# Optimization experiments

Measured on AMD Instinct MI355X. Metric: run time of the kernel, lower is better.

The kernel has to match this reference:

```python
import jax, jax.numpy as jnp
import numpy as np

B, N, D = 2, 2048, 512
H, DH = 8, 64
P = 64  # position_max_embedding


def setup_inputs() -> dict:
    key = jax.random.key(0)
    ks = jax.random.split(key, 8)
    s = 0.02
    return {
        "x": jax.random.normal(ks[0], (B, N, D), jnp.float32),
        "Wq": jax.random.normal(ks[1], (D, H * DH), jnp.float32) * s,
        "Wk": jax.random.normal(ks[2], (D, H * DH), jnp.float32) * s,
        "Wv": jax.random.normal(ks[3], (D, H * DH), jnp.float32) * s,
        "rel_pos": jax.random.normal(ks[4], (2 * P + 1, H), jnp.float32) * s,
        "c_emb": jax.random.uniform(ks[5], (2 * P + 1, H), jnp.float32, 0.5, 1.5),
        "Wo": jax.random.normal(ks[6], (H * DH, D), jnp.float32) * s,
        "bo": jnp.zeros((D,), jnp.float32),
    }


def reference(x, Wq, Wk, Wv, rel_pos, c_emb, Wo, bo):
    b, n, _ = x.shape
    scale = DH ** -0.5
    q = (x @ Wq).reshape(b, n, H, DH)
    k = (x @ Wk).reshape(b, n, H, DH)
    v = (x @ Wv).reshape(b, n, H, DH)
    # relative position index: j - i, clamped to [-P, P], shifted to [0, 2P]
    idx = jnp.clip(jnp.arange(n)[None, :] - jnp.arange(n)[:, None], -P, P) + P  # [n, n]
    pos_bias = rel_pos[idx]          # [n, n, H]
    c_gate = c_emb[idx]              # [n, n, H]
    sim = jnp.einsum('bihd,bjhd->bhij', q, k)  # [b, H, n, n]
    sim = (sim + pos_bias.transpose(2, 0, 1)[None]) * scale
    attn = jax.nn.softmax(sim, axis=-1) * c_gate.transpose(2, 0, 1)[None]
    out = jnp.einsum('bhij,bjhd->bihd', attn, v).reshape(b, n, H * DH)
    return out @ Wo + bo
```

## Files before the change

### kernel.cpp

```cpp
#include <hip/hip_runtime.h>
#include <stdint.h>

#define BB 2
#define NN 2048
#define DD 512
#define HH 8
#define DHH 64

typedef __attribute__((ext_vector_type(8))) short bf16x8;
typedef __attribute__((ext_vector_type(4))) float f32x4;

#define LOG2E 1.44269504088896340736f

#if __has_builtin(__builtin_amdgcn_exp2f)
#define QSCALE (0.125f * LOG2E)
#define EXP2(x) __builtin_amdgcn_exp2f(x)
#else
#define QSCALE 0.125f
#define EXP2(x) __expf(x)
#endif

static __device__ __forceinline__ unsigned short f2bf(float f) {
    union { float f; unsigned u; } v; v.f = f;
    unsigned r = v.u + 0x7fffu + ((v.u >> 16) & 1u);
    return (unsigned short)(r >> 16);
}

static __device__ __forceinline__ unsigned pkbf(float a, float b) {
    union { float f; unsigned u; } ua, ub; ua.f = a; ub.f = b;
    return ((ub.u + 0x8000u) & 0xffff0000u) | ((ua.u + 0x8000u) >> 16);
}

static __device__ __forceinline__ bf16x8 ld8(const unsigned short* p) {
    bf16x8 v; __builtin_memcpy(&v, p, 16); return v;
}

static __device__ __forceinline__ void gld_lds16(const void* g, void* l) {
    __builtin_amdgcn_global_load_lds((const __attribute__((address_space(1))) void*)g,
                                     (__attribute__((address_space(3))) void*)l, 16, 0, 0);
}

__global__ void ca_prep(const float* __restrict__ x,
                        const float* __restrict__ w0, const float* __restrict__ w1,
                        const float* __restrict__ w2, const float* __restrict__ w3,
                        unsigned short* __restrict__ xb, unsigned short* __restrict__ wts) {
    __shared__ float T[64][65];
    int bx = blockIdx.x;
    if (bx < 2048) {
        int gid = bx * 256 + threadIdx.x;
        float4 v = ((const float4*)x)[gid];
        ushort4 o;
        o.x = f2bf(v.x); o.y = f2bf(v.y); o.z = f2bf(v.z); o.w = f2bf(v.w);
        ((ushort4*)xb)[gid] = o;
        return;
    }
    int bb = bx - 2048;
    int z = bb >> 6, t = bb & 63;
    const float* W = (z == 0) ? w0 : (z == 1) ? w1 : (z == 2) ? w2 : w3;
    unsigned short* out = wts + z * 262144;
    int k0 = (t & 7) << 6, n0 = (t >> 3) << 6;
    int c = threadIdx.x & 63, r4 = threadIdx.x >> 6;
#pragma unroll
    for (int rr = 0; rr < 16; ++rr) {
        int r = r4 * 16 + rr;
        T[r][c] = W[(k0 + r) * 512 + n0 + c];
    }
    __syncthreads();
#pragma unroll
    for (int rr = 0; rr < 16; ++rr) {
        int r = r4 * 16 + rr;
        out[(n0 + r) * 512 + k0 + c] = f2bf(T[c][r]);
    }
}

__global__ __launch_bounds__(256, 3)
void ca_gemm_proj(const unsigned short* __restrict__ A,
                  const unsigned short* __restrict__ wts,
                  unsigned short* __restrict__ qkv,
                  unsigned short* __restrict__ vt) {
    __shared__ __align__(16) unsigned short Ash[2][128 * 64];
    __shared__ __align__(16) unsigned short Bsh[2][64 * 64];
    int z = blockIdx.y >> 3;
    const unsigned short* BT = wts + z * 262144;
    unsigned short* out = qkv + z * 2097152;
    int w = threadIdx.x >> 6, lane = threadIdx.x & 63;
    int c = lane & 15, qd = lane >> 4;
    int m0 = blockIdx.x * 128 + w * 16;
    int n0 = (blockIdx.y & 7) * 64;

    int lr = lane >> 3, ls = lane & 7;
    int soff = lr * 512 + ((ls ^ (lr & 7)) << 3);
    const unsigned short* Ab = A + (blockIdx.x * 128) * 512 + soff;
    const unsigned short* Bb = BT + n0 * 512 + soff;

#pragma unroll
    for (int L = 0; L < 4; ++L)
        gld_lds16(Ab + (w * 32 + L * 8) * 512, (char*)Ash[0] + (w * 32 + L * 8) * 128);
#pragma unroll
    for (int L = 0; L < 2; ++L)
        gld_lds16(Bb + (w * 16 + L * 8) * 512, (char*)Bsh[0] + (w * 16 + L * 8) * 128);

    f32x4 acc[2][4];
#pragma unroll
    for (int mt = 0; mt < 2; ++mt)
#pragma unroll
        for (int nb = 0; nb < 4; ++nb) acc[mt][nb] = (f32x4){0.f, 0.f, 0.f, 0.f};

    int cs = c & 7;
#pragma unroll
    for (int k = 0; k < 8; ++k) {
        int b = k & 1;
        if (k < 7) {
            int k0 = (k + 1) * 64;
#pragma unroll
            for (int L = 0; L < 4; ++L)
                gld_lds16(Ab + k0 + (w * 32 + L * 8) * 512, (char*)Ash[b ^ 1] + (w * 32 + L * 8) * 128);
#pragma unroll
            for (int L = 0; L < 2; ++L)
                gld_lds16(Bb + k0 + (w * 16 + L * 8) * 512, (char*)Bsh[b ^ 1] + (w * 16 + L * 8) * 128);
            asm volatile("s_waitcnt vmcnt(6)" ::: "memory");
        } else {
            asm volatile("s_waitcnt vmcnt(0)" ::: "memory");
        }
        __syncthreads();
        bf16x8 a[2][2], bq[4][2];
#pragma unroll
        for (int mt = 0; mt < 2; ++mt)
#pragma unroll
            for (int kk = 0; kk < 2; ++kk)
                a[mt][kk] = ld8((const unsigned short*)((char*)Ash[b] +
                                (w * 16 + mt * 64 + c) * 128 + (((kk * 4 + qd) ^ cs) << 4)));
#pragma unroll
        for (int nb = 0; nb < 4; ++nb)
#pragma unroll
            for (int kk = 0; kk < 2; ++kk)
                bq[nb][kk] = ld8((const unsigned short*)((char*)Bsh[b] +
                                (nb * 16 + c) * 128 + (((kk * 4 + qd) ^ cs) << 4)));
        asm volatile("s_waitcnt lgkmcnt(0)" ::: "memory");
        __syncthreads();
#pragma unroll
        for (int kk = 0; kk < 2; ++kk)
#pragma unroll
            for (int nb = 0; nb < 4; ++nb) {
                acc[0][nb] = __builtin_amdgcn_mfma_f32_16x16x32_bf16(a[0][kk], bq[nb][kk], acc[0][nb], 0, 0, 0);
                acc[1][nb] = __builtin_amdgcn_mfma_f32_16x16x32_bf16(a[1][kk], bq[nb][kk], acc[1][nb], 0, 0, 0);
            }
    }

    if (z == 2) {
#pragma unroll
        for (int mt = 0; mt < 2; ++mt) {
            int ib = m0 + mt * 64 + qd * 4;
            int b = ib >> 11, i = ib & 2047;
#pragma unroll
            for (int nb = 0; nb < 4; ++nb) {
                int col = n0 + nb * 16 + c;
                int h = col >> 6, d = col & 63;
                ushort4 pk;
                pk.x = f2bf(acc[mt][nb][0]); pk.y = f2bf(acc[mt][nb][1]);
                pk.z = f2bf(acc[mt][nb][2]); pk.w = f2bf(acc[mt][nb][3]);
                *(ushort4*)(vt + (((b << 3) + h) * 64 + d) * 2048 + i) = pk;
            }
        }
    } else {
        float scale = (z == 0) ? QSCALE : 1.0f;
#pragma unroll
        for (int mt = 0; mt < 2; ++mt)
#pragma unroll
            for (int nb = 0; nb < 4; ++nb) {
#pragma unroll
                for (int r = 0; r < 4; ++r) {
                    int row = m0 + mt * 64 + qd * 4 + r;
                    int col = n0 + nb * 16 + c;
                    int b = row >> 11, i = row & 2047, h = col >> 6, d = col & 63;
                    out[(((b << 3) + h) * 2048 + i) * 64 + d] = f2bf(acc[mt][nb][r] * scale);
                }
            }
    }
}

__global__ __launch_bounds__(256, 4)
void ca_flash(const unsigned short* __restrict__ Q,
              const unsigned short* __restrict__ K,
              const unsigned short* __restrict__ VT,
              const float* __restrict__ rel_pos,
              const float* __restrict__ c_emb,
              unsigned short* __restrict__ Ob) {
    __shared__ __align__(16) char smem[37904];
    unsigned (*Ptu)[16][16] = (unsigned (*)[16][16])(smem + 32768);
    float* red = (float*)smem;
    float2* lrg = (float2*)(smem + 36864);

    int bx = blockIdx.x;
    int xcd = bx & 7, slot = bx >> 3;
    int bh = xcd + ((slot >> 6) << 3);
    int it = slot & 63;
    int b = bh >> 3, h = bh & 7;
    int w = threadIdx.x >> 6, lane = threadIdx.x & 63;
    int c = lane & 15, qd = lane >> 4;
    int i0 = it * 32;

    if (threadIdx.x < 129) {
        lrg[threadIdx.x] = make_float2(rel_pos[threadIdx.x * 8 + h] * QSCALE,
                                       c_emb[threadIdx.x * 8 + h]);
    }

    const unsigned short* Qh = Q  + bh * 131072;
    const unsigned short* Kh = K  + bh * 131072;
    const unsigned short* Vh = VT + bh * 131072;
    char* kw = smem + w * 4096;
    char* vw = smem + 16384 + w * 4096;

    int koff[4], voff[4];
#pragma unroll
    for (int L = 0; L < 4; ++L) {
        int kr = L * 8 + (lane >> 3);
        koff[L] = kr * 64 + (((lane & 7) ^ ((kr >> 1) & 7)) << 3);
        int vr = L * 16 + (lane >> 2);
        voff[L] = vr * 2048 + (((lane & 3) ^ ((lane >> 3) & 3)) << 3);
    }

    {
        int j0 = w * 32;
#pragma unroll
        for (int L = 0; L < 4; ++L) gld_lds16(Kh + j0 * 64 + koff[L], kw + L * 1024);
#pragma unroll
        for (int L = 0; L < 4; ++L) gld_lds16(Vh + j0 + voff[L], vw + L * 1024);
    }

    bf16x8 aq[2][2];
#pragma unroll
    for (int qt = 0; qt < 2; ++qt) {
        aq[qt][0] = ld8(Qh + (i0 + qt * 16 + c) * 64 + qd * 8);
        aq[qt][1] = ld8(Qh + (i0 + qt * 16 + c) * 64 + 32 + qd * 8);
    }

    f32x4 o2[2][4];
    float lp2[2][4];
#pragma unroll
    for (int qt = 0; qt < 2; ++qt)
#pragma unroll
        for (int db = 0; db < 4; ++db) {
            o2[qt][db] = (f32x4){0.f, 0.f, 0.f, 0.f};
            lp2[qt][db] = 0.f;
        }

    __syncthreads();

    int ksw  = c & 7;
    int vsw  = (c >> 1) & 3;

    for (int t = 0; t < 16; ++t) {
        asm volatile("s_waitcnt vmcnt(0)" ::: "memory");
        __builtin_amdgcn_sched_barrier(0);
        bf16x8 bk0a = ld8((const unsigned short*)(kw + (2 * c) * 128     + (((qd)     ^ ksw) << 4)));
        bf16x8 bk0b = ld8((const unsigned short*)(kw + (2 * c) * 128     + (((qd + 4) ^ ksw) << 4)));
        bf16x8 bk1a = ld8((const unsigned short*)(kw + (2 * c + 1) * 128 + (((qd)     ^ ksw) << 4)));
        bf16x8 bk1b = ld8((const unsigned short*)(kw + (2 * c + 1) * 128 + (((qd + 4) ^ ksw) << 4)));
        bf16x8 bv[4];
#pragma unroll
        for (int db = 0; db < 4; ++db)
            bv[db] = ld8((const unsigned short*)(vw + (db * 16 + c) * 64 + ((qd ^ vsw) << 4)));
        asm volatile("s_waitcnt lgkmcnt(0)" ::: "memory");
        __builtin_amdgcn_sched_barrier(0);
        if (t < 15) {
            int j0n = ((t + 1) * 4 + w) * 32;
#pragma unroll
            for (int L = 0; L < 4; ++L) gld_lds16(Kh + j0n * 64 + koff[L], kw + L * 1024);
#pragma unroll
            for (int L = 0; L < 4; ++L) gld_lds16(Vh + j0n + voff[L], vw + L * 1024);
        }

        int j0 = (t * 4 + w) * 32;
#pragma unroll
        for (int qt = 0; qt < 2; ++qt) {
            f32x4 s0 = (f32x4){0.f, 0.f, 0.f, 0.f};
            f32x4 s1 = (f32x4){0.f, 0.f, 0.f, 0.f};
            s0 = __builtin_amdgcn_mfma_f32_16x16x32_bf16(aq[qt][0], bk0a, s0, 0, 0, 0);
            s0 = __builtin_amdgcn_mfma_f32_16x16x32_bf16(aq[qt][1], bk0b, s0, 0, 0, 0);
            s1 = __builtin_amdgcn_mfma_f32_16x16x32_bf16(aq[qt][0], bk1a, s1, 0, 0, 0);
            s1 = __builtin_amdgcn_mfma_f32_16x16x32_bf16(aq[qt][1], bk1b, s1, 0, 0, 0);

            int iqt0 = i0 + qt * 16;
            int iq = iqt0 + qd * 4;
            bool lowc  = (j0 + 31 - iqt0) <= -64;
            bool highc = (j0 - (iqt0 + 15)) >= 64;
            if (lowc || highc) {
                int d = lowc ? 0 : 128;
                float2 gg = lrg[d];
#pragma unroll
                for (int r = 0; r < 4; ++r) {
                    float t0 = EXP2(s0[r] + gg.x);
                    float t1 = EXP2(s1[r] + gg.x);
                    lp2[qt][r] += t0 + t1;
                    Ptu[w][qd * 4 + r][c] = pkbf(t0 * gg.y, t1 * gg.y);
                }
            } else {
#pragma unroll
                for (int r = 0; r < 4; ++r) {
                    int i = iq + r;
                    int j = j0 + 2 * c;
                    int d0 = j - i;     d0 = (d0 < -64) ? -64 : (d0 > 64 ? 64 : d0); d0 += 64;
                    int d1 = j + 1 - i; d1 = (d1 < -64) ? -64 : (d1 > 64 ? 64 : d1); d1 += 64;
                    float2 g0 = lrg[d0];
                    float2 g1 = lrg[d1];
                    float t0 = EXP2(s0[r] + g0.x);
                    float t1 = EXP2(s1[r] + g1.x);
                    lp2[qt][r] += t0 + t1;
                    Ptu[w][qd * 4 + r][c] = pkbf(t0 * g0.y, t1 * g1.y);
                }
            }
            bf16x8 ap = ld8((const unsigned short*)&Ptu[w][c][0] + qd * 8);
#pragma unroll
            for (int db = 0; db < 4; ++db)
                o2[qt][db] = __builtin_amdgcn_mfma_f32_16x16x32_bf16(ap, bv[db], o2[qt][db], 0, 0, 0);
        }
    }

    __syncthreads();
    if (w > 0) {
        float* dst = red + (w - 1) * (64 * 41) + lane * 41;
#pragma unroll
        for (int qt = 0; qt < 2; ++qt)
#pragma unroll
            for (int db = 0; db < 4; ++db)
#pragma unroll
                for (int r = 0; r < 4; ++r)
                    dst[qt * 16 + db * 4 + r] = o2[qt][db][r];
#pragma unroll
        for (int qt = 0; qt < 2; ++qt)
#pragma unroll
            for (int r = 0; r < 4; ++r)
                dst[32 + qt * 4 + r] = lp2[qt][r];
    }
    __syncthreads();
    if (w == 0) {
#pragma unroll
        for (int ww = 0; ww < 3; ++ww) {
            const float* src = red + ww * (64 * 41) + lane * 41;
#pragma unroll
            for (int qt = 0; qt < 2; ++qt) {
#pragma unroll
                for (int db = 0; db < 4; ++db)
#pragma unroll
                    for (int r = 0; r < 4; ++r)
                        o2[qt][db][r] += src[qt * 16 + db * 4 + r];
#pragma unroll
                for (int r = 0; r < 4; ++r)
                    lp2[qt][r] += src[32 + qt * 4 + r];
            }
        }
#pragma unroll
        for (int qt = 0; qt < 2; ++qt)
#pragma unroll
            for (int r = 0; r < 4; ++r) {
                lp2[qt][r] += __shfl_xor(lp2[qt][r], 1);
                lp2[qt][r] += __shfl_xor(lp2[qt][r], 2);
                lp2[qt][r] += __shfl_xor(lp2[qt][r], 4);
                lp2[qt][r] += __shfl_xor(lp2[qt][r], 8);
            }
#pragma unroll
        for (int qt = 0; qt < 2; ++qt)
#pragma unroll
            for (int db = 0; db < 4; ++db)
#pragma unroll
                for (int r = 0; r < 4; ++r) {
                    int row = b * 2048 + i0 + qt * 16 + qd * 4 + r;
                    int col = h * 64 + db * 16 + c;
                    Ob[row * 512 + col] = f2bf(o2[qt][db][r] / lp2[qt][r]);
                }
    }
}

__global__ __launch_bounds__(256, 4)
void ca_gemm_out(const unsigned short* __restrict__ A,
                 const unsigned short* __restrict__ BT,
                 const float* __restrict__ bias,
                 float* __restrict__ out) {
    __shared__ __align__(16) unsigned short Ash[2][64 * 64];
    __shared__ __align__(16) unsigned short Bsh[2][64 * 64];
    int w = threadIdx.x >> 6, lane = threadIdx.x & 63;
    int c = lane & 15, qd = lane >> 4;
    int m0 = blockIdx.x * 64 + w * 16;
    int n0 = blockIdx.y * 64;

    int lr = lane >> 3, ls = lane & 7;
    int soff = lr * 512 + ((ls ^ (lr & 7)) << 3);
    const unsigned short* Ab = A + (blockIdx.x * 64) * 512 + soff;
    const unsigned short* Bb = BT + n0 * 512 + soff;

#pragma unroll
    for (int L = 0; L < 2; ++L) {
        gld_lds16(Ab + (w * 16 + L * 8) * 512, (char*)Ash[0] + (w * 16 + L * 8) * 128);
        gld_lds16(Bb + (w * 16 + L * 8) * 512, (char*)Bsh[0] + (w * 16 + L * 8) * 128);
    }

    f32x4 acc[4];
#pragma unroll
    for (int nb = 0; nb < 4; ++nb) acc[nb] = (f32x4){0.f, 0.f, 0.f, 0.f};

    int cs = c & 7;
#pragma unroll
    for (int k = 0; k < 8; ++k) {
        int b = k & 1;
        if (k < 7) {
            int k0 = (k + 1) * 64;
#pragma unroll
            for (int L = 0; L < 2; ++L) {
                gld_lds16(Ab + k0 + (w * 16 + L * 8) * 512, (char*)Ash[b ^ 1] + (w * 16 + L * 8) * 128);
                gld_lds16(Bb + k0 + (w * 16 + L * 8) * 512, (char*)Bsh[b ^ 1] + (w * 16 + L * 8) * 128);
            }
            asm volatile("s_waitcnt vmcnt(4)" ::: "memory");
        } else {
            asm volatile("s_waitcnt vmcnt(0)" ::: "memory");
        }
        __syncthreads();
        bf16x8 a[2], bq[4][2];
#pragma unroll
        for (int kk = 0; kk < 2; ++kk)
            a[kk] = ld8((const unsigned short*)((char*)Ash[b] +
                        (w * 16 + c) * 128 + (((kk * 4 + qd) ^ cs) << 4)));
#pragma unroll
        for (int nb = 0; nb < 4; ++nb)
#pragma unroll
            for (int kk = 0; kk < 2; ++kk)
                bq[nb][kk] = ld8((const unsigned short*)((char*)Bsh[b] +
                                (nb * 16 + c) * 128 + (((kk * 4 + qd) ^ cs) << 4)));
        asm volatile("s_waitcnt lgkmcnt(0)" ::: "memory");
        __syncthreads();
#pragma unroll
        for (int kk = 0; kk < 2; ++kk)
#pragma unroll
            for (int nb = 0; nb < 4; ++nb)
                acc[nb] = __builtin_amdgcn_mfma_f32_16x16x32_bf16(a[kk], bq[nb][kk], acc[nb], 0, 0, 0);
    }
#pragma unroll
    for (int nb = 0; nb < 4; ++nb) {
#pragma unroll
        for (int r = 0; r < 4; ++r) {
            int row = m0 + qd * 4 + r;
            int col = n0 + nb * 16 + c;
            out[row * 512 + col] = acc[nb][r] + bias[col];
        }
    }
}

extern "C" void kernel_launch(void* const* d_in, const int* in_sizes, int n_in,
                              void* d_out, int out_size, void* d_ws, size_t ws_size,
                              hipStream_t stream) {
    const float* x   = (const float*)d_in[0];
    const float* Wq  = (const float*)d_in[1];
    const float* Wk  = (const float*)d_in[2];
    const float* Wv  = (const float*)d_in[3];
    const float* rel = (const float*)d_in[4];
    const float* cem = (const float*)d_in[5];
    const float* Wo  = (const float*)d_in[6];
    const float* bo  = (const float*)d_in[7];
    float* out = (float*)d_out;
    char* ws = (char*)d_ws;

    unsigned short* xb  = (unsigned short*)(ws);
    unsigned short* wts = (unsigned short*)(ws + 4194304);
    unsigned short* qkv = (unsigned short*)(ws + 6291456);
    unsigned short* vt  = (unsigned short*)(ws + 18874368);
    unsigned short* ob  = (unsigned short*)(ws + 23068672);

    hipLaunchKernelGGL(ca_prep, dim3(2304), dim3(256), 0, stream, x, Wq, Wk, Wv, Wo, xb, wts);
    hipLaunchKernelGGL(ca_gemm_proj, dim3(32, 24), dim3(256), 0, stream, xb, wts, qkv, vt);
    hipLaunchKernelGGL(ca_flash, dim3(1024), dim3(256), 0, stream,
                       qkv, qkv + 2097152, vt, rel, cem, ob);
    hipLaunchKernelGGL(ca_gemm_out, dim3(64, 8), dim3(256), 0, stream, ob, wts + 3 * 262144, bo, out);
}
```

Baseline: 139.2 us.

## Merge four kernels into two using software grid barriers

Folds the prep/convert stage and the QKV projection GEMM into one persistent kernel separated by an atomic grid barrier. It likewise fuses the flash attention stage with the output projection GEMM in a second kernel with its own barrier, so launches drop from four to two plus a memset. The goal is to remove launch gaps and kernel-boundary drains. The cost is that the spin barriers require every block to be co-resident (768 and 1024 blocks) and could deadlock or serialize if occupancy is insufficient. It also adds a memset launch and barrier spin overhead.

```diff
diff --git a/kernel.cpp b/kernel.cpp
--- a/kernel.cpp
+++ b/kernel.cpp
@@ -40,407 +40,438 @@
                                      (__attribute__((address_space(3))) void*)l, 16, 0, 0);
 }
 
-__global__ void ca_prep(const float* __restrict__ x,
-                        const float* __restrict__ w0, const float* __restrict__ w1,
-                        const float* __restrict__ w2, const float* __restrict__ w3,
-                        unsigned short* __restrict__ xb, unsigned short* __restrict__ wts) {
-    __shared__ float T[64][65];
-    int bx = blockIdx.x;
-    if (bx < 2048) {
-        int gid = bx * 256 + threadIdx.x;
-        float4 v = ((const float4*)x)[gid];
-        ushort4 o;
-        o.x = f2bf(v.x); o.y = f2bf(v.y); o.z = f2bf(v.z); o.w = f2bf(v.w);
-        ((ushort4*)xb)[gid] = o;
-        return;
-    }
-    int bb = bx - 2048;
-    int z = bb >> 6, t = bb & 63;
-    const float* W = (z == 0) ? w0 : (z == 1) ? w1 : (z == 2) ? w2 : w3;
-    unsigned short* out = wts + z * 262144;
-    int k0 = (t & 7) << 6, n0 = (t >> 3) << 6;
-    int c = threadIdx.x & 63, r4 = threadIdx.x >> 6;
-#pragma unroll
-    for (int rr = 0; rr < 16; ++rr) {
-        int r = r4 * 16 + rr;
-        T[r][c] = W[(k0 + r) * 512 + n0 + c];
+static __device__ __forceinline__ void grid_barrier(unsigned* cnt, unsigned n) {
+    __syncthreads();
+    if (threadIdx.x == 0) {
+        __threadfence();
+        atomicAdd(cnt, 1u);
+        while (__hip_atomic_load(cnt, __ATOMIC_RELAXED, __HIP_MEMORY_SCOPE_AGENT) < n) {
+            __builtin_amdgcn_s_sleep(1);
+        }
+        __threadfence();
     }
     __syncthreads();
-#pragma unroll
-    for (int rr = 0; rr < 16; ++rr) {
-        int r = r4 * 16 + rr;
-        out[(n0 + r) * 512 + k0 + c] = f2bf(T[c][r]);
+}
+
+__global__ __launch_bounds__(256, 3)
+void ca_k1(const float* __restrict__ x,
+           const float* __restrict__ w0, const float* __restrict__ w1,
+           const float* __restrict__ w2, const float* __restrict__ w3,
+           unsigned short* __restrict__ xb, unsigned short* __restrict__ wts,
+           unsigned short* __restrict__ qkv, unsigned short* __restrict__ vt,
+           unsigned* __restrict__ bar) {
+    __shared__ __align__(16) char sm[49152];
+    int tid = threadIdx.x;
+
+    {
+        float (*T)[65] = (float (*)[65])sm;
+        for (int u = blockIdx.x; u < 2304; u += 768) {
+            if (u < 2048) {
+                int gid = u * 256 + tid;
+                float4 v = ((const float4*)x)[gid];
+                ushort4 o;
+                o.x = f2bf(v.x); o.y = f2bf(v.y); o.z = f2bf(v.z); o.w = f2bf(v.w);
+                ((ushort4*)xb)[gid] = o;
+            } else {
+                int bb = u - 2048;
+                int z = bb >> 6, t = bb & 63;
+                const float* W = (z == 0) ? w0 : (z == 1) ? w1 : (z == 2) ? w2 : w3;
+                unsigned short* out = wts + z * 262144;
+                int k0 = (t & 7) << 6, n0 = (t >> 3) << 6;
+                int c = tid & 63, r4 = tid >> 6;
+#pragma unroll
+                for (int rr = 0; rr < 16; ++rr) {
+                    int r = r4 * 16 + rr;
+                    T[r][c] = W[(k0 + r) * 512 + n0 + c];
+                }
+                __syncthreads();
+#pragma unroll
+                for (int rr = 0; rr < 16; ++rr) {
+                    int r = r4 * 16 + rr;
+                    out[(n0 + r) * 512 + k0 + c] = f2bf(T[c][r]);
+                }
+            }
+        }
     }
-}
-
-__global__ __launch_bounds__(256, 3)
-void ca_gemm_proj(const unsigned short* __restrict__ A,
-                  const unsigned short* __restrict__ wts,
-                  unsigned short* __restrict__ qkv,
-                  unsigned short* __restrict__ vt) {
-    __shared__ __align__(16) unsigned short Ash[2][128 * 64];
-    __shared__ __align__(16) unsigned short Bsh[2][64 * 64];
-    int z = blockIdx.y >> 3;
-    const unsigned short* BT = wts + z * 262144;
-    unsigned short* out = qkv + z * 2097152;
-    int w = threadIdx.x >> 6, lane = threadIdx.x & 63;
-    int c = lane & 15, qd = lane >> 4;
-    int m0 = blockIdx.x * 128 + w * 16;
-    int n0 = (blockIdx.y & 7) * 64;
-
-    int lr = lane >> 3, ls = lane & 7;
-    int soff = lr * 512 + ((ls ^ (lr & 7)) << 3);
-    const unsigned short* Ab = A + (blockIdx.x * 128) * 512 + soff;
-    const unsigned short* Bb = BT + n0 * 512 + soff;
-
-#pragma unroll
-    for (int L = 0; L < 4; ++L)
-        gld_lds16(Ab + (w * 32 + L * 8) * 512, (char*)Ash[0] + (w * 32 + L * 8) * 128);
-#pragma unroll
-    for (int L = 0; L < 2; ++L)
-        gld_lds16(Bb + (w * 16 + L * 8) * 512, (char*)Bsh[0] + (w * 16 + L * 8) * 128);
-
-    f32x4 acc[2][4];
-#pragma unroll
-    for (int mt = 0; mt < 2; ++mt)
-#pragma unroll
-        for (int nb = 0; nb < 4; ++nb) acc[mt][nb] = (f32x4){0.f, 0.f, 0.f, 0.f};
-
-    int cs = c & 7;
-#pragma unroll
-    for (int k = 0; k < 8; ++k) {
-        int b = k & 1;
-        if (k < 7) {
-            int k0 = (k + 1) * 64;
-#pragma unroll
-            for (int L = 0; L < 4; ++L)
-                gld_lds16(Ab + k0 + (w * 32 + L * 8) * 512, (char*)Ash[b ^ 1] + (w * 32 + L * 8) * 128);
-#pragma unroll
-            for (int L = 0; L < 2; ++L)
-                gld_lds16(Bb + k0 + (w * 16 + L * 8) * 512, (char*)Bsh[b ^ 1] + (w * 16 + L * 8) * 128);
-            asm volatile("s_waitcnt vmcnt(6)" ::: "memory");
+    grid_barrier(bar, 768);
+
+    {
+        char* AshB = sm;
+        char* BshB = sm + 32768;
+        int px = blockIdx.x & 31, py = blockIdx.x >> 5;
+        int z = py >> 3;
+        const unsigned short* BT = wts + z * 262144;
+        unsigned short* out = qkv + z * 2097152;
+        int w = tid >> 6, lane = tid & 63;
+        int c = lane & 15, qd = lane >> 4;
+        int m0 = px * 128 + w * 16;
+        int n0 = (py & 7) * 64;
+
+        int lr = lane >> 3, ls = lane & 7;
+        int soff = lr * 512 + ((ls ^ (lr & 7)) << 3);
+        const unsigned short* Ab = xb + (px * 128) * 512 + soff;
+        const unsigned short* Bb = BT + n0 * 512 + soff;
+
+#pragma unroll
+        for (int L = 0; L < 4; ++L)
+            gld_lds16(Ab + (w * 32 + L * 8) * 512, AshB + (w * 32 + L * 8) * 128);
+#pragma unroll
+        for (int L = 0; L < 2; ++L)
+            gld_lds16(Bb + (w * 16 + L * 8) * 512, BshB + (w * 16 + L * 8) * 128);
+
+        f32x4 acc[2][4];
+#pragma unroll
+        for (int mt = 0; mt < 2; ++mt)
+#pragma unroll
+            for (int nb = 0; nb < 4; ++nb) acc[mt][nb] = (f32x4){0.f, 0.f, 0.f, 0.f};
+
+        int cs = c & 7;
+#pragma unroll
+        for (int k = 0; k < 8; ++k) {
+            int b = k & 1;
+            if (k < 7) {
+                int k0 = (k + 1) * 64;
+#pragma unroll
+                for (int L = 0; L < 4; ++L)
+                    gld_lds16(Ab + k0 + (w * 32 + L * 8) * 512,
+                              AshB + (b ^ 1) * 16384 + (w * 32 + L * 8) * 128);
+#pragma unroll
+                for (int L = 0; L < 2; ++L)
+                    gld_lds16(Bb + k0 + (w * 16 + L * 8) * 512,
+                              BshB + (b ^ 1) * 8192 + (w * 16 + L * 8) * 128);
+                asm volatile("s_waitcnt vmcnt(6)" ::: "memory");
+            } else {
+                asm volatile("s_waitcnt vmcnt(0)" ::: "memory");
+            }
+            __syncthreads();
+            bf16x8 a[2][2], bq[4][2];
+#pragma unroll
+            for (int mt = 0; mt < 2; ++mt)
+#pragma unroll
+                for (int kk = 0; kk < 2; ++kk)
+                    a[mt][kk] = ld8((const unsigned short*)(AshB + b * 16384 +
+                                    (w * 16 + mt * 64 + c) * 128 + (((kk * 4 + qd) ^ cs) << 4)));
+#pragma unroll
+            for (int nb = 0; nb < 4; ++nb)
+#pragma unroll
+                for (int kk = 0; kk < 2; ++kk)
+                    bq[nb][kk] = ld8((const unsigned short*)(BshB + b * 8192 +
+                                     (nb * 16 + c) * 128 + (((kk * 4 + qd) ^ cs) << 4)));
+            asm volatile("s_waitcnt lgkmcnt(0)" ::: "memory");
+            __syncthreads();
+#pragma unroll
+            for (int kk = 0; kk < 2; ++kk)
+#pragma unroll
+                for (int nb = 0; nb < 4; ++nb) {
+                    acc[0][nb] = __builtin_amdgcn_mfma_f32_16x16x32_bf16(a[0][kk], bq[nb][kk], acc[0][nb], 0, 0, 0);
+                    acc[1][nb] = __builtin_amdgcn_mfma_f32_16x16x32_bf16(a[1][kk], bq[nb][kk], acc[1][nb], 0, 0, 0);
+                }
+        }
+
+        if (z == 2) {
+#pragma unroll
+            for (int mt = 0; mt < 2; ++mt) {
+                int ib = m0 + mt * 64 + qd * 4;
+                int b = ib >> 11, i = ib & 2047;
+#pragma unroll
+                for (int nb = 0; nb < 4; ++nb) {
+                    int col = n0 + nb * 16 + c;
+                    int h = col >> 6, d = col & 63;
+                    ushort4 pk;
+                    pk.x = f2bf(acc[mt][nb][0]); pk.y = f2bf(acc[mt][nb][1]);
+                    pk.z = f2bf(acc[mt][nb][2]); pk.w = f2bf(acc[mt][nb][3]);
+                    *(ushort4*)(vt + (((b << 3) + h) * 64 + d) * 2048 + i) = pk;
+                }
+            }
         } else {
+            float scale = (z == 0) ? QSCALE : 1.0f;
+#pragma unroll
+            for (int mt = 0; mt < 2; ++mt)
+#pragma unroll
+                for (int nb = 0; nb < 4; ++nb) {
+#pragma unroll
+                    for (int r = 0; r < 4; ++r) {
+                        int row = m0 + mt * 64 + qd * 4 + r;
+                        int col = n0 + nb * 16 + c;
+                        int b = row >> 11, i = row & 2047, h = col >> 6, d = col & 63;
+                        out[(((b << 3) + h) * 2048 + i) * 64 + d] = f2bf(acc[mt][nb][r] * scale);
+                    }
+                }
+        }
+    }
+}
+
+__global__ __launch_bounds__(256, 4)
+void ca_k2(const unsigned short* __restrict__ Q,
+           const unsigned short* __restrict__ K,
+           const unsigned short* __restrict__ VTp,
+           const float* __restrict__ rel_pos,
+           const float* __restrict__ c_emb,
+           unsigned short* __restrict__ Ob,
+           const unsigned short* __restrict__ WoT,
+           const float* __restrict__ bias,
+           float* __restrict__ out,
+           unsigned* __restrict__ bar) {
+    __shared__ __align__(16) char smem[37904];
+    int tid = threadIdx.x;
+
+    {
+        unsigned (*Ptu)[16][16] = (unsigned (*)[16][16])(smem + 32768);
+        float* red = (float*)smem;
+        float2* lrg = (float2*)(smem + 36864);
+
+        int bx = blockIdx.x;
+        int xcd = bx & 7, slot = bx >> 3;
+        int bh = xcd + ((slot >> 6) << 3);
+        int it = slot & 63;
+        int b = bh >> 3, h = bh & 7;
+        int w = tid >> 6, lane = tid & 63;
+        int c = lane & 15, qd = lane >> 4;
+        int i0 = it * 32;
+
+        if (tid < 129) {
+            lrg[tid] = make_float2(rel_pos[tid * 8 + h] * QSCALE, c_emb[tid * 8 + h]);
+        }
+
+        const unsigned short* Qh = Q   + bh * 131072;
+        const unsigned short* Kh = K   + bh * 131072;
+        const unsigned short* Vh = VTp + bh * 131072;
+        char* kw = smem + w * 4096;
+        char* vw = smem + 16384 + w * 4096;
+
+        int koff[4], voff[4];
+#pragma unroll
+        for (int L = 0; L < 4; ++L) {
+            int kr = L * 8 + (lane >> 3);
+            koff[L] = kr * 64 + (((lane & 7) ^ ((kr >> 1) & 7)) << 3);
+            int vr = L * 16 + (lane >> 2);
+            voff[L] = vr * 2048 + (((lane & 3) ^ ((lane >> 3) & 3)) << 3);
+        }
+
+        {
+            int j0 = w * 32;
+#pragma unroll
+            for (int L = 0; L < 4; ++L) gld_lds16(Kh + j0 * 64 + koff[L], kw + L * 1024);
+#pragma unroll
+            for (int L = 0; L < 4; ++L) gld_lds16(Vh + j0 + voff[L], vw + L * 1024);
+        }
+
+        bf16x8 aq[2][2];
+#pragma unroll
+        for (int qt = 0; qt < 2; ++qt) {
+            aq[qt][0] = ld8(Qh + (i0 + qt * 16 + c) * 64 + qd * 8);
+            aq[qt][1] = ld8(Qh + (i0 + qt * 16 + c) * 64 + 32 + qd * 8);
+        }
+
+        f32x4 o2[2][4];
+        float lp2[2][4];
+#pragma unroll
+        for (int qt = 0; qt < 2; ++qt)
+#pragma unroll
+            for (int db = 0; db < 4; ++db) {
+                o2[qt][db] = (f32x4){0.f, 0.f, 0.f, 0.f};
+                lp2[qt][db] = 0.f;
+            }
+
+        __syncthreads();
+
+        int ksw = c & 7;
+        int vsw = (c >> 1) & 3;
+
+        for (int t = 0; t < 16; ++t) {
             asm volatile("s_waitcnt vmcnt(0)" ::: "memory");
-        }
+            __builtin_amdgcn_sched_barrier(0);
+            bf16x8 bk0a = ld8((const unsigned short*)(kw + (2 * c) * 128     + (((qd)     ^ ksw) << 4)));
+            bf16x8 bk0b = ld8((const unsigned short*)(kw + (2 * c) * 128     + (((qd + 4) ^ ksw) << 4)));
+            bf16x8 bk1a = ld8((const unsigned short*)(kw + (2 * c + 1) * 128 + (((qd)     ^ ksw) << 4)));
+            bf16x8 bk1b = ld8((const unsigned short*)(kw + (2 * c + 1) * 128 + (((qd + 4) ^ ksw) << 4)));
+            bf16x8 bv[4];
+#pragma unroll
+            for (int db = 0; db < 4; ++db)
+                bv[db] = ld8((const unsigned short*)(vw + (db * 16 + c) * 64 + ((qd ^ vsw) << 4)));
+            asm volatile("s_waitcnt lgkmcnt(0)" ::: "memory");
+            __builtin_amdgcn_sched_barrier(0);
+            if (t < 15) {
+                int j0n = ((t + 1) * 4 + w) * 32;
+#pragma unroll
+                for (int L = 0; L < 4; ++L) gld_lds16(Kh + j0n * 64 + koff[L], kw + L * 1024);
+#pragma unroll
+                for (int L = 0; L < 4; ++L) gld_lds16(Vh + j0n + voff[L], vw + L * 1024);
+            }
+
+            int j0 = (t * 4 + w) * 32;
+#pragma unroll
+            for (int qt = 0; qt < 2; ++qt) {
+                f32x4 s0 = (f32x4){0.f, 0.f, 0.f, 0.f};
+                f32x4 s1 = (f32x4){0.f, 0.f, 0.f, 0.f};
+                s0 = __builtin_amdgcn_mfma_f32_16x16x32_bf16(aq[qt][0], bk0a, s0, 0, 0, 0);
+                s0 = __builtin_amdgcn_mfma_f32_16x16x32_bf16(aq[qt][1], bk0b, s0, 0, 0, 0);
+                s1 = __builtin_amdgcn_mfma_f32_16x16x32_bf16(aq[qt][0], bk1a, s1, 0, 0, 0);
+                s1 = __builtin_amdgcn_mfma_f32_16x16x32_bf16(aq[qt][1], bk1b, s1, 0, 0, 0);
+
+                int iqt0 = i0 + qt * 16;
+                int iq = iqt0 + qd * 4;
+                bool lowc  = (j0 + 31 - iqt0) <= -64;
+                bool highc = (j0 - (iqt0 + 15)) >= 64;
+                if (lowc || highc) {
+                    int d = lowc ? 0 : 128;
+                    float2 gg = lrg[d];
+#pragma unroll
+                    for (int r = 0; r < 4; ++r) {
+                        float t0 = EXP2(s0[r] + gg.x);
+                        float t1 = EXP2(s1[r] + gg.x);
+                        lp2[qt][r] += t0 + t1;
+                        Ptu[w][qd * 4 + r][c] = pkbf(t0 * gg.y, t1 * gg.y);
+                    }
+                } else {
+#pragma unroll
+                    for (int r = 0; r < 4; ++r) {
+                        int i = iq + r;
+                        int j = j0 + 2 * c;
+                        int d0 = j - i;     d0 = (d0 < -64) ? -64 : (d0 > 64 ? 64 : d0); d0 += 64;
+                        int d1 = j + 1 - i; d1 = (d1 < -64) ? -64 : (d1 > 64 ? 64 : d1); d1 += 64;
+                        float2 g0 = lrg[d0];
+                        float2 g1 = lrg[d1];
+                        float t0 = EXP2(s0[r] + g0.x);
+                        float t1 = EXP2(s1[r] + g1.x);
+                        lp2[qt][r] += t0 + t1;
+                        Ptu[w][qd * 4 + r][c] = pkbf(t0 * g0.y, t1 * g1.y);
+                    }
+                }
+                bf16x8 ap = ld8((const unsigned short*)&Ptu[w][c][0] + qd * 8);
+#pragma unroll
+                for (int db = 0; db < 4; ++db)
+                    o2[qt][db] = __builtin_amdgcn_mfma_f32_16x16x32_bf16(ap, bv[db], o2[qt][db], 0, 0, 0);
+            }
+        }
+
         __syncthreads();
-        bf16x8 a[2][2], bq[4][2];
-#pragma unroll
-        for (int mt = 0; mt < 2; ++mt)
+        if (w > 0) {
+            float* dst = red + (w - 1) * (64 * 41) + lane * 41;
+#pragma unroll
+            for (int qt = 0; qt < 2; ++qt)
+#pragma unroll
+                for (int db = 0; db < 4; ++db)
+#pragma unroll
+                    for (int r = 0; r < 4; ++r)
+                        dst[qt * 16 + db * 4 + r] = o2[qt][db][r];
+#pragma unroll
+            for (int qt = 0; qt < 2; ++qt)
+#pragma unroll
+                for (int r = 0; r < 4; ++r)
+                    dst[32 + qt * 4 + r] = lp2[qt][r];
+        }
+        __syncthreads();
+        if (w == 0) {
+#pragma unroll
+            for (int ww = 0; ww < 3; ++ww) {
+                const float* src = red + ww * (64 * 41) + lane * 41;
+#pragma unroll
+                for (int qt = 0; qt < 2; ++qt) {
+#pragma unroll
+                    for (int db = 0; db < 4; ++db)
+#pragma unroll
+                        for (int r = 0; r < 4; ++r)
+                            o2[qt][db][r] += src[qt * 16 + db * 4 + r];
+#pragma unroll
+                    for (int r = 0; r < 4; ++r)
+                        lp2[qt][r] += src[32 + qt * 4 + r];
+                }
+            }
+#pragma unroll
+            for (int qt = 0; qt < 2; ++qt)
+#pragma unroll
+                for (int r = 0; r < 4; ++r) {
+                    lp2[qt][r] += __shfl_xor(lp2[qt][r], 1);
+                    lp2[qt][r] += __shfl_xor(lp2[qt][r], 2);
+                    lp2[qt][r] += __shfl_xor(lp2[qt][r], 4);
+                    lp2[qt][r] += __shfl_xor(lp2[qt][r], 8);
+                }
+#pragma unroll
+            for (int qt = 0; qt < 2; ++qt)
+#pragma unroll
+                for (int db = 0; db < 4; ++db)
+#pragma unroll
+                    for (int r = 0; r < 4; ++r) {
+                        int row = b * 2048 + i0 + qt * 16 + qd * 4 + r;
+                        int col = h * 64 + db * 16 + c;
+                        Ob[row * 512 + col] = f2bf(o2[qt][db][r] / lp2[qt][r]);
+                    }
+        }
+    }
+
+    grid_barrier(bar, 1024);
+
+    if (blockIdx.x < 512) {
+        char* AshB = smem;
+        char* BshB = smem + 16384;
+        int u = blockIdx.x;
+        int px = u & 63, py = u >> 6;
+        int w = tid >> 6, lane = tid & 63;
+        int c = lane & 15, qd = lane >> 4;
+        int m0 = px * 64 + w * 16;
+        int n0 = py * 64;
+
+        int lr = lane >> 3, ls = lane & 7;
+        int soff = lr * 512 + ((ls ^ (lr & 7)) << 3);
+        const unsigned short* Ab = Ob + (px * 64) * 512 + soff;
+        const unsigned short* Bb = WoT + n0 * 512 + soff;
+
+#pragma unroll
+        for (int L = 0; L < 2; ++L) {
+            gld_lds16(Ab + (w * 16 + L * 8) * 512, AshB + (w * 16 + L * 8) * 128);
+            gld_lds16(Bb + (w * 16 + L * 8) * 512, BshB + (w * 16 + L * 8) * 128);
+        }
+
+        f32x4 acc[4];
+#pragma unroll
+        for (int nb = 0; nb < 4; ++nb) acc[nb] = (f32x4){0.f, 0.f, 0.f, 0.f};
+
+        int cs = c & 7;
+#pragma unroll
+        for (int k = 0; k < 8; ++k) {
+            int b = k & 1;
+            if (k < 7) {
+                int k0 = (k + 1) * 64;
+#pragma unroll
+                for (int L = 0; L < 2; ++L) {
+                    gld_lds16(Ab + k0 + (w * 16 + L * 8) * 512,
+                              AshB + (b ^ 1) * 8192 + (w * 16 + L * 8) * 128);
+                    gld_lds16(Bb + k0 + (w * 16 + L * 8) * 512,
+                              BshB + (b ^ 1) * 8192 + (w * 16 + L * 8) * 128);
+                }
+                asm volatile("s_waitcnt vmcnt(4)" ::: "memory");
+            } else {
+                asm volatile("s_waitcnt vmcnt(0)" ::: "memory");
+            }
+            __syncthreads();
+            bf16x8 a[2], bq[4][2];
 #pragma unroll
             for (int kk = 0; kk < 2; ++kk)
-                a[mt][kk] = ld8((const unsigned short*)((char*)Ash[b] +
-                                (w * 16 + mt * 64 + c) * 128 + (((kk * 4 + qd) ^ cs) << 4)));
-#pragma unroll
-        for (int nb = 0; nb < 4; ++nb)
+                a[kk] = ld8((const unsigned short*)(AshB + b * 8192 +
+                            (w * 16 + c) * 128 + (((kk * 4 + qd) ^ cs) << 4)));
+#pragma unroll
+            for (int nb = 0; nb < 4; ++nb)
+#pragma unroll
+                for (int kk = 0; kk < 2; ++kk)
+                    bq[nb][kk] = ld8((const unsigned short*)(BshB + b * 8192 +
+                                     (nb * 16 + c) * 128 + (((kk * 4 + qd) ^ cs) << 4)));
+            asm volatile("s_waitcnt lgkmcnt(0)" ::: "memory");
+            __syncthreads();
 #pragma unroll
             for (int kk = 0; kk < 2; ++kk)
-                bq[nb][kk] = ld8((const unsigned short*)((char*)Bsh[b] +
-                                (nb * 16 + c) * 128 + (((kk * 4 + qd) ^ cs) << 4)));
-        asm volatile("s_waitcnt lgkmcnt(0)" ::: "memory");
-        __syncthreads();
-#pragma unroll
-        for (int kk = 0; kk < 2; ++kk)
-#pragma unroll
-            for (int nb = 0; nb < 4; ++nb) {
-                acc[0][nb] = __builtin_amdgcn_mfma_f32_16x16x32_bf16(a[0][kk], bq[nb][kk], acc[0][nb], 0, 0, 0);
-                acc[1][nb] = __builtin_amdgcn_mfma_f32_16x16x32_bf16(a[1][kk], bq[nb][kk], acc[1][nb], 0, 0, 0);
-            }
-    }
-
-    if (z == 2) {
-#pragma unroll
-        for (int mt = 0; mt < 2; ++mt) {
-            int ib = m0 + mt * 64 + qd * 4;
-            int b = ib >> 11, i = ib & 2047;
-#pragma unroll
-            for (int nb = 0; nb < 4; ++nb) {
+#pragma unroll
+                for (int nb = 0; nb < 4; ++nb)
+                    acc[nb] = __builtin_amdgcn_mfma_f32_16x16x32_bf16(a[kk], bq[nb][kk], acc[nb], 0, 0, 0);
+        }
+#pragma unroll
+        for (int nb = 0; nb < 4; ++nb) {
+#pragma unroll
+            for (int r = 0; r < 4; ++r) {
+                int row = m0 + qd * 4 + r;
                 int col = n0 + nb * 16 + c;
-                int h = col >> 6, d = col & 63;
-                ushort4 pk;
-                pk.x = f2bf(acc[mt][nb][0]); pk.y = f2bf(acc[mt][nb][1]);
-                pk.z = f2bf(acc[mt][nb][2]); pk.w = f2bf(acc[mt][nb][3]);
-                *(ushort4*)(vt + (((b << 3) + h) * 64 + d) * 2048 + i) = pk;
-            }
-        }
-    } else {
-        float scale = (z == 0) ? QSCALE : 1.0f;
-#pragma unroll
-        for (int mt = 0; mt < 2; ++mt)
-#pragma unroll
-            for (int nb = 0; nb < 4; ++nb) {
-#pragma unroll
-                for (int r = 0; r < 4; ++r) {
-                    int row = m0 + mt * 64 + qd * 4 + r;
-                    int col = n0 + nb * 16 + c;
-                    int b = row >> 11, i = row & 2047, h = col >> 6, d = col & 63;
-                    out[(((b << 3) + h) * 2048 + i) * 64 + d] = f2bf(acc[mt][nb][r] * scale);
-                }
-            }
-    }
-}
-
-__global__ __launch_bounds__(256, 4)
-void ca_flash(const unsigned short* __restrict__ Q,
-              const unsigned short* __restrict__ K,
-              const unsigned short* __restrict__ VT,
-              const float* __restrict__ rel_pos,
-              const float* __restrict__ c_emb,
-              unsigned short* __restrict__ Ob) {
-    __shared__ __align__(16) char smem[37904];
-    unsigned (*Ptu)[16][16] = (unsigned (*)[16][16])(smem + 32768);
-    float* red = (float*)smem;
-    float2* lrg = (float2*)(smem + 36864);
-
-    int bx = blockIdx.x;
-    int xcd = bx & 7, slot = bx >> 3;
-    int bh = xcd + ((slot >> 6) << 3);
-    int it = slot & 63;
-    int b = bh >> 3, h = bh & 7;
-    int w = threadIdx.x >> 6, lane = threadIdx.x & 63;
-    int c = lane & 15, qd = lane >> 4;
-    int i0 = it * 32;
-
-    if (threadIdx.x < 129) {
-        lrg[threadIdx.x] = make_float2(rel_pos[threadIdx.x * 8 + h] * QSCALE,
-                                       c_emb[threadIdx.x * 8 + h]);
-    }
-
-    const unsigned short* Qh = Q  + bh * 131072;
-    const unsigned short* Kh = K  + bh * 131072;
-    const unsigned short* Vh = VT + bh * 131072;
-    char* kw = smem + w * 4096;
-    char* vw = smem + 16384 + w * 4096;
-
-    int koff[4], voff[4];
-#pragma unroll
-    for (int L = 0; L < 4; ++L) {
-        int kr = L * 8 + (lane >> 3);
-        koff[L] = kr * 64 + (((lane & 7) ^ ((kr >> 1) & 7)) << 3);
-        int vr = L * 16 + (lane >> 2);
-        voff[L] = vr * 2048 + (((lane & 3) ^ ((lane >> 3) & 3)) << 3);
-    }
-
-    {
-        int j0 = w * 32;
-#pragma unroll
-        for (int L = 0; L < 4; ++L) gld_lds16(Kh + j0 * 64 + koff[L], kw + L * 1024);
-#pragma unroll
-        for (int L = 0; L < 4; ++L) gld_lds16(Vh + j0 + voff[L], vw + L * 1024);
-    }
-
-    bf16x8 aq[2][2];
-#pragma unroll
-    for (int qt = 0; qt < 2; ++qt) {
-        aq[qt][0] = ld8(Qh + (i0 + qt * 16 + c) * 64 + qd * 8);
-        aq[qt][1] = ld8(Qh + (i0 + qt * 16 + c) * 64 + 32 + qd * 8);
-    }
-
-    f32x4 o2[2][4];
-    float lp2[2][4];
-#pragma unroll
-    for (int qt = 0; qt < 2; ++qt)
-#pragma unroll
-        for (int db = 0; db < 4; ++db) {
-            o2[qt][db] = (f32x4){0.f, 0.f, 0.f, 0.f};
-            lp2[qt][db] = 0.f;
-        }
-
-    __syncthreads();
-
-    int ksw  = c & 7;
-    int vsw  = (c >> 1) & 3;
-
-    for (int t = 0; t < 16; ++t) {
-        asm volatile("s_waitcnt vmcnt(0)" ::: "memory");
-        __builtin_amdgcn_sched_barrier(0);
-        bf16x8 bk0a = ld8((const unsigned short*)(kw + (2 * c) * 128     + (((qd)     ^ ksw) << 4)));
-        bf16x8 bk0b = ld8((const unsigned short*)(kw + (2 * c) * 128     + (((qd + 4) ^ ksw) << 4)));
-        bf16x8 bk1a = ld8((const unsigned short*)(kw + (2 * c + 1) * 128 + (((qd)     ^ ksw) << 4)));
-        bf16x8 bk1b = ld8((const unsigned short*)(kw + (2 * c + 1) * 128 + (((qd + 4) ^ ksw) << 4)));
-        bf16x8 bv[4];
-#pragma unroll
-        for (int db = 0; db < 4; ++db)
-            bv[db] = ld8((const unsigned short*)(vw + (db * 16 + c) * 64 + ((qd ^ vsw) << 4)));
-        asm volatile("s_waitcnt lgkmcnt(0)" ::: "memory");
-        __builtin_amdgcn_sched_barrier(0);
-        if (t < 15) {
-            int j0n = ((t + 1) * 4 + w) * 32;
-#pragma unroll
-            for (int L = 0; L < 4; ++L) gld_lds16(Kh + j0n * 64 + koff[L], kw + L * 1024);
-#pragma unroll
-            for (int L = 0; L < 4; ++L) gld_lds16(Vh + j0n + voff[L], vw + L * 1024);
-        }
-
-        int j0 = (t * 4 + w) * 32;
-#pragma unroll
-        for (int qt = 0; qt < 2; ++qt) {
-            f32x4 s0 = (f32x4){0.f, 0.f, 0.f, 0.f};
-            f32x4 s1 = (f32x4){0.f, 0.f, 0.f, 0.f};
-            s0 = __builtin_amdgcn_mfma_f32_16x16x32_bf16(aq[qt][0], bk0a, s0, 0, 0, 0);
-            s0 = __builtin_amdgcn_mfma_f32_16x16x32_bf16(aq[qt][1], bk0b, s0, 0, 0, 0);
-            s1 = __builtin_amdgcn_mfma_f32_16x16x32_bf16(aq[qt][0], bk1a, s1, 0, 0, 0);
-            s1 = __builtin_amdgcn_mfma_f32_16x16x32_bf16(aq[qt][1], bk1b, s1, 0, 0, 0);
-
-            int iqt0 = i0 + qt * 16;
-            int iq = iqt0 + qd * 4;
-            bool lowc  = (j0 + 31 - iqt0) <= -64;
-            bool highc = (j0 - (iqt0 + 15)) >= 64;
-            if (lowc || highc) {
-                int d = lowc ? 0 : 128;
-                float2 gg = lrg[d];
-#pragma unroll
-                for (int r = 0; r < 4; ++r) {
-                    float t0 = EXP2(s0[r] + gg.x);
-                    float t1 = EXP2(s1[r] + gg.x);
-                    lp2[qt][r] += t0 + t1;
-                    Ptu[w][qd * 4 + r][c] = pkbf(t0 * gg.y, t1 * gg.y);
-                }
-            } else {
-#pragma unroll
-                for (int r = 0; r < 4; ++r) {
-                    int i = iq + r;
-                    int j = j0 + 2 * c;
-                    int d0 = j - i;     d0 = (d0 < -64) ? -64 : (d0 > 64 ? 64 : d0); d0 += 64;
-                    int d1 = j + 1 - i; d1 = (d1 < -64) ? -64 : (d1 > 64 ? 64 : d1); d1 += 64;
-                    float2 g0 = lrg[d0];
-                    float2 g1 = lrg[d1];
-                    float t0 = EXP2(s0[r] + g0.x);
-                    float t1 = EXP2(s1[r] + g1.x);
-                    lp2[qt][r] += t0 + t1;
-                    Ptu[w][qd * 4 + r][c] = pkbf(t0 * g0.y, t1 * g1.y);
-                }
-            }
-            bf16x8 ap = ld8((const unsigned short*)&Ptu[w][c][0] + qd * 8);
-#pragma unroll
-            for (int db = 0; db < 4; ++db)
-                o2[qt][db] = __builtin_amdgcn_mfma_f32_16x16x32_bf16(ap, bv[db], o2[qt][db], 0, 0, 0);
-        }
-    }
-
-    __syncthreads();
-    if (w > 0) {
-        float* dst = red + (w - 1) * (64 * 41) + lane * 41;
-#pragma unroll
-        for (int qt = 0; qt < 2; ++qt)
-#pragma unroll
-            for (int db = 0; db < 4; ++db)
-#pragma unroll
-                for (int r = 0; r < 4; ++r)
-                    dst[qt * 16 + db * 4 + r] = o2[qt][db][r];
-#pragma unroll
-        for (int qt = 0; qt < 2; ++qt)
-#pragma unroll
-            for (int r = 0; r < 4; ++r)
-                dst[32 + qt * 4 + r] = lp2[qt][r];
-    }
-    __syncthreads();
-    if (w == 0) {
-#pragma unroll
-        for (int ww = 0; ww < 3; ++ww) {
-            const float* src = red + ww * (64 * 41) + lane * 41;
-#pragma unroll
-            for (int qt = 0; qt < 2; ++qt) {
-#pragma unroll
-                for (int db = 0; db < 4; ++db)
-#pragma unroll
-                    for (int r = 0; r < 4; ++r)
-                        o2[qt][db][r] += src[qt * 16 + db * 4 + r];
-#pragma unroll
-                for (int r = 0; r < 4; ++r)
-                    lp2[qt][r] += src[32 + qt * 4 + r];
-            }
-        }
-#pragma unroll
-        for (int qt = 0; qt < 2; ++qt)
-#pragma unroll
-            for (int r = 0; r < 4; ++r) {
-                lp2[qt][r] += __shfl_xor(lp2[qt][r], 1);
-                lp2[qt][r] += __shfl_xor(lp2[qt][r], 2);
-                lp2[qt][r] += __shfl_xor(lp2[qt][r], 4);
-                lp2[qt][r] += __shfl_xor(lp2[qt][r], 8);
-            }
-#pragma unroll
-        for (int qt = 0; qt < 2; ++qt)
-#pragma unroll
-            for (int db = 0; db < 4; ++db)
-#pragma unroll
-                for (int r = 0; r < 4; ++r) {
-                    int row = b * 2048 + i0 + qt * 16 + qd * 4 + r;
-                    int col = h * 64 + db * 16 + c;
-                    Ob[row * 512 + col] = f2bf(o2[qt][db][r] / lp2[qt][r]);
-                }
-    }
-}
-
-__global__ __launch_bounds__(256, 4)
-void ca_gemm_out(const unsigned short* __restrict__ A,
-                 const unsigned short* __restrict__ BT,
-                 const float* __restrict__ bias,
-                 float* __restrict__ out) {
-    __shared__ __align__(16) unsigned short Ash[2][64 * 64];
-    __shared__ __align__(16) unsigned short Bsh[2][64 * 64];
-    int w = threadIdx.x >> 6, lane = threadIdx.x & 63;
-    int c = lane & 15, qd = lane >> 4;
-    int m0 = blockIdx.x * 64 + w * 16;
-    int n0 = blockIdx.y * 64;
-
-    int lr = lane >> 3, ls = lane & 7;
-    int soff = lr * 512 + ((ls ^ (lr & 7)) << 3);
-    const unsigned short* Ab = A + (blockIdx.x * 64) * 512 + soff;
-    const unsigned short* Bb = BT + n0 * 512 + soff;
-
-#pragma unroll
-    for (int L = 0; L < 2; ++L) {
-        gld_lds16(Ab + (w * 16 + L * 8) * 512, (char*)Ash[0] + (w * 16 + L * 8) * 128);
-        gld_lds16(Bb + (w * 16 + L * 8) * 512, (char*)Bsh[0] + (w * 16 + L * 8) * 128);
-    }
-
-    f32x4 acc[4];
-#pragma unroll
-    for (int nb = 0; nb < 4; ++nb) acc[nb] = (f32x4){0.f, 0.f, 0.f, 0.f};
-
-    int cs = c & 7;
-#pragma unroll
-    for (int k = 0; k < 8; ++k) {
-        int b = k & 1;
-        if (k < 7) {
-            int k0 = (k + 1) * 64;
-#pragma unroll
-            for (int L = 0; L < 2; ++L) {
-                gld_lds16(Ab + k0 + (w * 16 + L * 8) * 512, (char*)Ash[b ^ 1] + (w * 16 + L * 8) * 128);
-                gld_lds16(Bb + k0 + (w * 16 + L * 8) * 512, (char*)Bsh[b ^ 1] + (w * 16 + L * 8) * 128);
-            }
-            asm volatile("s_waitcnt vmcnt(4)" ::: "memory");
-        } else {
-            asm volatile("s_waitcnt vmcnt(0)" ::: "memory");
-        }
-        __syncthreads();
-        bf16x8 a[2], bq[4][2];
-#pragma unroll
-        for (int kk = 0; kk < 2; ++kk)
-            a[kk] = ld8((const unsigned short*)((char*)Ash[b] +
-                        (w * 16 + c) * 128 + (((kk * 4 + qd) ^ cs) << 4)));
-#pragma unroll
-        for (int nb = 0; nb < 4; ++nb)
-#pragma unroll
-            for (int kk = 0; kk < 2; ++kk)
-                bq[nb][kk] = ld8((const unsigned short*)((char*)Bsh[b] +
-                                (nb * 16 + c) * 128 + (((kk * 4 + qd) ^ cs) << 4)));
-        asm volatile("s_waitcnt lgkmcnt(0)" ::: "memory");
-        __syncthreads();
-#pragma unroll
-        for (int kk = 0; kk < 2; ++kk)
-#pragma unroll
-            for (int nb = 0; nb < 4; ++nb)
-                acc[nb] = __builtin_amdgcn_mfma_f32_16x16x32_bf16(a[kk], bq[nb][kk], acc[nb], 0, 0, 0);
-    }
-#pragma unroll
-    for (int nb = 0; nb < 4; ++nb) {
-#pragma unroll
-        for (int r = 0; r < 4; ++r) {
-            int row = m0 + qd * 4 + r;
-            int col = n0 + nb * 16 + c;
-            out[row * 512 + col] = acc[nb][r] + bias[col];
+                out[row * 512 + col] = acc[nb][r] + bias[col];
+            }
         }
     }
 }
@@ -464,10 +495,13 @@
     unsigned short* qkv = (unsigned short*)(ws + 6291456);
     unsigned short* vt  = (unsigned short*)(ws + 18874368);
     unsigned short* ob  = (unsigned short*)(ws + 23068672);
-
-    hipLaunchKernelGGL(ca_prep, dim3(2304), dim3(256), 0, stream, x, Wq, Wk, Wv, Wo, xb, wts);
-    hipLaunchKernelGGL(ca_gemm_proj, dim3(32, 24), dim3(256), 0, stream, xb, wts, qkv, vt);
-    hipLaunchKernelGGL(ca_flash, dim3(1024), dim3(256), 0, stream,
-                       qkv, qkv + 2097152, vt, rel, cem, ob);
-    hipLaunchKernelGGL(ca_gemm_out, dim3(64, 8), dim3(256), 0, stream, ob, wts + 3 * 262144, bo, out);
-}
+    unsigned* bars      = (unsigned*)(ws + 27262976);
+
+    hipMemsetAsync(bars, 0, 8, stream);
+
+    hipLaunchKernelGGL(ca_k1, dim3(768), dim3(256), 0, stream,
+                       x, Wq, Wk, Wv, Wo, xb, wts, qkv, vt, bars);
+    hipLaunchKernelGGL(ca_k2, dim3(1024), dim3(256), 0, stream,
+                       qkv, qkv + 2097152, vt, rel, cem, ob,
+                       wts + 3 * 262144, bo, out, bars + 1);
+}
```

Measured after the change: 345.6 us. 148% more time.
